# Optimization experiments

Measured on AMD Instinct MI355X. Metric: run time of the kernel, lower is better.

Reference implementation:

```python
import jax, jax.numpy as jnp
import numpy as np

HEADS = 8
DIM_HEAD = 64
SCALE = DIM_HEAD ** -0.5


def setup_inputs() -> dict:
    key = jax.random.key(0)
    ks = jax.random.split(key, 8)
    B, Nq, Nk, D = 4, 1024, 2048, 512
    inner = HEADS * DIM_HEAD  # 512
    x = jax.random.normal(ks[0], (B, Nq, D), dtype=jnp.float32)
    context = jax.random.normal(ks[1], (B, Nk, D), dtype=jnp.float32)
    bias = jax.random.normal(ks[2], (B, Nq, Nk), dtype=jnp.float32)
    s = D ** -0.5
    Wq = jax.random.normal(ks[3], (inner, D), dtype=jnp.float32) * s
    Wk = jax.random.normal(ks[4], (inner, D), dtype=jnp.float32) * s
    Wv = jax.random.normal(ks[5], (inner, D), dtype=jnp.float32) * s
    Wo = jax.random.normal(ks[6], (D, inner), dtype=jnp.float32) * s
    bo = jnp.zeros((D,), dtype=jnp.float32)
    return {"x": x, "context": context, "bias": bias,
            "Wq": Wq, "Wk": Wk, "Wv": Wv, "Wo": Wo, "bo": bo}


def reference(x, context, bias, Wq, Wk, Wv, Wo, bo):
    B, Nq, _ = x.shape
    # torch Linear: y = x @ W.T ; reshape (h d) -> b h n d
    q = (x @ Wq.T).reshape(B, Nq, HEADS, DIM_HEAD).transpose(0, 2, 1, 3)
    k = (context @ Wk.T).reshape(B, -1, HEADS, DIM_HEAD).transpose(0, 2, 1, 3)
    v = (context @ Wv.T).reshape(B, -1, HEADS, DIM_HEAD).transpose(0, 2, 1, 3)
    # explicit-score fallback path (bias supplied)
    scores = jnp.einsum('bhqd,bhkd->bhqk', q, k) * SCALE
    scores = scores + bias[:, None, :, :]  # 3D bias -> (B,1,Nq,Nk)
    attn = jax.nn.softmax(scores, axis=-1)
    out = jnp.einsum('bhqk,bhkd->bhqd', attn, v)
    out = out.transpose(0, 2, 1, 3).reshape(B, Nq, HEADS * DIM_HEAD)
    return out @ Wo.T + bo
```

## Files before the change

### kernel.cpp

```cpp
#include <hip/hip_runtime.h>

#define H 8
#define DH 64
#define NQ 1024
#define NK 2048
#define DIN 512
#define B 4
#define KSPLIT 2
#define KRANGE (NK / KSPLIT)
#define KTILES (KRANGE / 64)
#define BHNQ (B * H * NQ)

typedef __bf16 bf16;
typedef __bf16 bf16x8 __attribute__((ext_vector_type(8)));
typedef __bf16 bf16x4 __attribute__((ext_vector_type(4)));
typedef float floatx4 __attribute__((ext_vector_type(4)));

__device__ inline void gload16(const void* g, void* l) {
  __builtin_amdgcn_global_load_lds(
      (const __attribute__((address_space(1))) void*)g,
      (__attribute__((address_space(3))) void*)l, 16, 0, 0);
}

__global__ void cvt_all(const float* __restrict__ x, const float* __restrict__ ctx,
                        const float* __restrict__ wq, const float* __restrict__ wk,
                        const float* __restrict__ wv, const float* __restrict__ wo,
                        bf16* xb, bf16* cb, bf16* wqb, bf16* wkb, bf16* wvb, bf16* wob) {
  long i = ((long)blockIdx.x * 256 + threadIdx.x) * 4;
  const float* s; bf16* d; long o;
  if (i < 2097152)      { s = x;   d = xb;  o = i; }
  else if (i < 6291456) { s = ctx; d = cb;  o = i - 2097152; }
  else if (i < 6553600) { s = wq;  d = wqb; o = i - 6291456; }
  else if (i < 6815744) { s = wk;  d = wkb; o = i - 6553600; }
  else if (i < 7077888) { s = wv;  d = wvb; o = i - 6815744; }
  else                  { s = wo;  d = wob; o = i - 7077888; }
  float4 f = *(const float4*)(s + o);
  bf16x4 v = { (bf16)f.x, (bf16)f.y, (bf16)f.z, (bf16)f.w };
  *(bf16x4*)(d + o) = v;
}

__global__ __launch_bounds__(256) void gemm_qkv(
    const bf16* __restrict__ xb, const bf16* __restrict__ cb,
    const bf16* __restrict__ wqb, const bf16* __restrict__ wkb, const bf16* __restrict__ wvb,
    bf16* __restrict__ qb, bf16* __restrict__ kb, bf16* __restrict__ vtb) {
  const int which = blockIdx.z;
  if (which == 0 && blockIdx.y >= 64) return;
  const bf16* A = (which == 0) ? xb : cb;
  const bf16* W = (which == 0) ? wqb : ((which == 1) ? wkb : wvb);
  bf16* outb = (which == 0) ? qb : ((which == 1) ? kb : vtb);
  const int logT = (which == 0) ? 10 : 11;
  const float scale = (which == 0) ? 0.125f : 1.0f;
  const bool vmode = (which == 2);

  __shared__ bf16 Al[2][64 * 32];
  __shared__ bf16 Bl[2][128 * 32];
  const int t = threadIdx.x;
  const int lane = t & 63, w = t >> 6;
  const int ln = lane & 15, quad = lane >> 4;
  const int wm = (w >> 1) * 32, wn = (w & 1) * 64;
  const int rowBase = blockIdx.y * 64;
  const int colBase = blockIdx.x * 128;

  floatx4 acc[2][4] = {};
  const int rA = t >> 2, oA = (t & 3) * 8;
  const int c0 = t, c1 = t + 256;
  const int rB0 = c0 >> 2, oB0 = (c0 & 3) * 8;
  const int rB1 = c1 >> 2, oB1 = (c1 & 3) * 8;
  const bf16* Ab = A + (size_t)rowBase * DIN;
  const bf16* Wb = W + (size_t)colBase * DIN;

  gload16(Ab + (size_t)rA * DIN + oA, &Al[0][t * 8]);
  gload16(Wb + (size_t)rB0 * DIN + oB0, &Bl[0][c0 * 8]);
  gload16(Wb + (size_t)rB1 * DIN + oB1, &Bl[0][c1 * 8]);
  __syncthreads();

  for (int k0 = 0; k0 < DIN; k0 += 32) {
    const int cur = (k0 >> 5) & 1, nxt = cur ^ 1;
    if (k0 + 32 < DIN) {
      gload16(Ab + (size_t)rA * DIN + k0 + 32 + oA, &Al[nxt][t * 8]);
      gload16(Wb + (size_t)rB0 * DIN + k0 + 32 + oB0, &Bl[nxt][c0 * 8]);
      gload16(Wb + (size_t)rB1 * DIN + k0 + 32 + oB1, &Bl[nxt][c1 * 8]);
    }
    bf16x8 af[2], bfr[4];
#pragma unroll
    for (int i = 0; i < 2; i++)
      af[i] = *(const bf16x8*)&Al[cur][(wm + i * 16 + ln) * 32 + quad * 8];
#pragma unroll
    for (int j = 0; j < 4; j++)
      bfr[j] = *(const bf16x8*)&Bl[cur][(wn + j * 16 + ln) * 32 + quad * 8];
    if (!vmode) {
#pragma unroll
      for (int i = 0; i < 2; i++)
#pragma unroll
        for (int j = 0; j < 4; j++)
          acc[i][j] = __builtin_amdgcn_mfma_f32_16x16x32_bf16(af[i], bfr[j], acc[i][j], 0, 0, 0);
    } else {
#pragma unroll
      for (int i = 0; i < 2; i++)
#pragma unroll
        for (int j = 0; j < 4; j++)
          acc[i][j] = __builtin_amdgcn_mfma_f32_16x16x32_bf16(bfr[j], af[i], acc[i][j], 0, 0, 0);
    }
    __syncthreads();
  }

  const int T = 1 << logT;
#pragma unroll
  for (int i = 0; i < 2; i++)
#pragma unroll
    for (int j = 0; j < 4; j++)
#pragma unroll
      for (int r = 0; r < 4; r++) {
        if (!vmode) {
          const int m = rowBase + wm + i * 16 + quad * 4 + r;
          const int n = colBase + wn + j * 16 + ln;
          const float v = acc[i][j][r] * scale;
          const int bb = m >> logT, tok = m & (T - 1);
          const int hh = n >> 6, d = n & 63;
          outb[((((size_t)(bb * H + hh)) << logT) + tok) * DH + d] = (bf16)v;
        } else {
          const int dg = colBase + wn + j * 16 + quad * 4 + r;
          const int m = rowBase + wm + i * 16 + ln;
          const int bb = m >> logT, tok = m & (T - 1);
          const int hh = dg >> 6, d = dg & 63;
          outb[(((size_t)(bb * H + hh) * DH + d) << logT) + tok] = (bf16)acc[i][j][r];
        }
      }
}

__global__ __launch_bounds__(256) void attn_fwd(
    const bf16* __restrict__ q, const bf16* __restrict__ k,
    const bf16* __restrict__ vt, const float* __restrict__ bias,
    float* __restrict__ op0, float* __restrict__ op1, float* __restrict__ lpart) {
  __shared__ bf16 KL[64 * 64];
  __shared__ bf16 VL[64 * 64];
  __shared__ bf16 Pl[4][2][16 * 64];
  const int tid = threadIdx.x;
  const int lane = tid & 63, w = tid >> 6;
  const int ln = lane & 15, quad = lane >> 4;
  const int hh = blockIdx.y;
  const int b = blockIdx.z >> 1, ks = blockIdx.z & 1;
  const int q0 = blockIdx.x * 128;
  const int k0 = ks * KRANGE;
  const size_t bh = (size_t)b * H + hh;
  const bf16* qp = q + bh * NQ * DH;
  const bf16* kp = k + bh * NK * DH;
  const bf16* vp = vt + bh * DH * NK;
  const float* bp = bias + ((size_t)b * NQ + q0 + w * 32 + quad * 4) * NK + ln;

  bf16x8 qf[2][2];
#pragma unroll
  for (int s = 0; s < 2; s++)
#pragma unroll
    for (int kc = 0; kc < 2; kc++)
      qf[s][kc] = *(const bf16x8*)(qp + (size_t)(q0 + w * 32 + s * 16 + ln) * DH + kc * 32 + quad * 8);

  floatx4 o[2][4] = {};
  floatx4 lac[2] = {};
  const bf16x8 ones = {(bf16)1.f, (bf16)1.f, (bf16)1.f, (bf16)1.f,
                       (bf16)1.f, (bf16)1.f, (bf16)1.f, (bf16)1.f};
  constexpr float L2E = 1.44269504f;
  constexpr float OFF = 34.6246810f;

  for (int tt = 0; tt < KTILES; tt++) {
    const int nk0 = k0 + tt * 64;
#pragma unroll
    for (int s = 0; s < 2; s++) {
      const int i = s * 256 + tid;
      const int sr = i >> 3, sc = (i & 7) ^ (sr & 7);
      gload16(kp + (size_t)(nk0 + sr) * DH + sc * 8, &KL[i * 8]);
      gload16(vp + (size_t)sr * NK + nk0 + sc * 8, &VL[i * 8]);
    }
    float bc[2][4][4];
#pragma unroll
    for (int s = 0; s < 2; s++)
#pragma unroll
      for (int j = 0; j < 4; j++)
#pragma unroll
        for (int r = 0; r < 4; r++)
          bc[s][j][r] = bp[(size_t)(s * 16 + r) * NK + nk0 + j * 16];
    __syncthreads();

    floatx4 s4[2][4];
#pragma unroll
    for (int s = 0; s < 2; s++)
#pragma unroll
      for (int j = 0; j < 4; j++) {
        s4[s][j][0] = bc[s][j][0]; s4[s][j][1] = bc[s][j][1];
        s4[s][j][2] = bc[s][j][2]; s4[s][j][3] = bc[s][j][3];
      }
#pragma unroll
    for (int j = 0; j < 4; j++)
#pragma unroll
      for (int kc = 0; kc < 2; kc++) {
        const int kr = j * 16 + ln;
        bf16x8 kf = *(const bf16x8*)&KL[kr * 64 + (((kc * 4 + quad) ^ (kr & 7)) * 8)];
        s4[0][j] = __builtin_amdgcn_mfma_f32_16x16x32_bf16(qf[0][kc], kf, s4[0][j], 0, 0, 0);
        s4[1][j] = __builtin_amdgcn_mfma_f32_16x16x32_bf16(qf[1][kc], kf, s4[1][j], 0, 0, 0);
      }

#pragma unroll
    for (int s = 0; s < 2; s++)
#pragma unroll
      for (int j = 0; j < 4; j++)
#pragma unroll
        for (int r = 0; r < 4; r++)
          s4[s][j][r] = exp2f(fmaf(s4[s][j][r], L2E, -OFF));

#pragma unroll
    for (int s = 0; s < 2; s++)
#pragma unroll
      for (int j = 0; j < 4; j++)
#pragma unroll
        for (int r = 0; r < 4; r++) {
          const int m = quad * 4 + r;
          Pl[w][s][m * 64 + (((j * 2 + (ln >> 3)) ^ (m & 7)) * 8) + (ln & 7)] = (bf16)s4[s][j][r];
        }
    asm volatile("s_waitcnt lgkmcnt(0)" ::: "memory");
    bf16x8 pf[2][2];
#pragma unroll
    for (int s = 0; s < 2; s++)
#pragma unroll
      for (int kc = 0; kc < 2; kc++)
        pf[s][kc] = *(const bf16x8*)&Pl[w][s][ln * 64 + (((kc * 4 + quad) ^ (ln & 7)) * 8)];

#pragma unroll
    for (int s = 0; s < 2; s++)
#pragma unroll
      for (int kc = 0; kc < 2; kc++)
        lac[s] = __builtin_amdgcn_mfma_f32_16x16x32_bf16(pf[s][kc], ones, lac[s], 0, 0, 0);

#pragma unroll
    for (int jn = 0; jn < 4; jn++)
#pragma unroll
      for (int kc = 0; kc < 2; kc++) {
        const int vr = jn * 16 + ln;
        bf16x8 vf = *(const bf16x8*)&VL[vr * 64 + (((kc * 4 + quad) ^ (vr & 7)) * 8)];
        o[0][jn] = __builtin_amdgcn_mfma_f32_16x16x32_bf16(pf[0][kc], vf, o[0][jn], 0, 0, 0);
        o[1][jn] = __builtin_amdgcn_mfma_f32_16x16x32_bf16(pf[1][kc], vf, o[1][jn], 0, 0, 0);
      }
    __syncthreads();
  }

#pragma unroll
  for (int s = 0; s < 2; s++) {
    float* op = (ks ? op1 : op0) +
                ((size_t)b * NQ + q0 + w * 32 + s * 16 + quad * 4) * DIN + hh * 64 + ln;
#pragma unroll
    for (int jn = 0; jn < 4; jn++)
#pragma unroll
      for (int r = 0; r < 4; r++)
        op[(size_t)r * DIN + jn * 16] = o[s][jn][r];
    if (ln == 0) {
      float4 lv = {lac[s][0], lac[s][1], lac[s][2], lac[s][3]};
      *(float4*)&lpart[((size_t)ks * B * H + b * H + hh) * NQ + q0 + w * 32 + s * 16 + quad * 4] = lv;
    }
  }
}

__global__ __launch_bounds__(256) void gemm_out(
    const float* __restrict__ op0, const float* __restrict__ op1,
    const float* __restrict__ lp, const bf16* __restrict__ W,
    float* __restrict__ outf, const float* __restrict__ bo) {
  __shared__ bf16 Al[2][64 * 32];
  __shared__ bf16 Bl[2][128 * 32];
  const int t = threadIdx.x;
  const int lane = t & 63, w = t >> 6;
  const int ln = lane & 15, quad = lane >> 4;
  const int wm = (w >> 1) * 32, wn = (w & 1) * 64;
  const int rowBase = blockIdx.y * 64;
  const int colBase = blockIdx.x * 128;

  floatx4 acc[2][4] = {};
  const int rA = t >> 2, oA = (t & 3) * 8;
  const int c0 = t, c1 = t + 256;
  const int rB0 = c0 >> 2, oB0 = (c0 & 3) * 8;
  const int rB1 = c1 >> 2, oB1 = (c1 & 3) * 8;
  const int m0 = rowBase + rA;
  const bf16* Wb = W + (size_t)colBase * DIN;

  float linv0[8];
#pragma unroll
  for (int h = 0; h < 8; h++) {
    const int i0 = ((m0 >> 10) * H + h) * NQ + (m0 & 1023);
    linv0[h] = 1.0f / (lp[i0] + lp[BHNQ + i0]);
  }

#define STAGE_A(K0V, BUF)                                                      \
  {                                                                            \
    const float sA = linv0[(K0V) >> 6];                                        \
    const float* pa0 = op0 + (size_t)m0 * DIN + (K0V) + oA;                    \
    const float* pa1 = op1 + (size_t)m0 * DIN + (K0V) + oA;                    \
    float4 xa = *(const float4*)pa0, xb2 = *(const float4*)(pa0 + 4);          \
    float4 ya = *(const float4*)pa1, yb = *(const float4*)(pa1 + 4);           \
    bf16x8 v0 = {(bf16)((xa.x + ya.x) * sA), (bf16)((xa.y + ya.y) * sA),       \
                 (bf16)((xa.z + ya.z) * sA), (bf16)((xa.w + ya.w) * sA),       \
                 (bf16)((xb2.x + yb.x) * sA), (bf16)((xb2.y + yb.y) * sA),     \
                 (bf16)((xb2.z + yb.z) * sA), (bf16)((xb2.w + yb.w) * sA)};    \
    *(bf16x8*)&Al[BUF][t * 8] = v0;                                            \
  }

  STAGE_A(0, 0);
  gload16(Wb + (size_t)rB0 * DIN + oB0, &Bl[0][c0 * 8]);
  gload16(Wb + (size_t)rB1 * DIN + oB1, &Bl[0][c1 * 8]);
  __syncthreads();

#pragma unroll
  for (int kk = 0; kk < 16; kk++) {
    const int cur = kk & 1, nxt = cur ^ 1;
    if (kk < 15) {
      const int k1 = (kk + 1) * 32;
      STAGE_A(k1, nxt);
      gload16(Wb + (size_t)rB0 * DIN + k1 + oB0, &Bl[nxt][c0 * 8]);
      gload16(Wb + (size_t)rB1 * DIN + k1 + oB1, &Bl[nxt][c1 * 8]);
    }
    bf16x8 af[2], bfr[4];
#pragma unroll
    for (int i = 0; i < 2; i++)
      af[i] = *(const bf16x8*)&Al[cur][(wm + i * 16 + ln) * 32 + quad * 8];
#pragma unroll
    for (int j = 0; j < 4; j++)
      bfr[j] = *(const bf16x8*)&Bl[cur][(wn + j * 16 + ln) * 32 + quad * 8];
#pragma unroll
    for (int i = 0; i < 2; i++)
#pragma unroll
      for (int j = 0; j < 4; j++)
        acc[i][j] = __builtin_amdgcn_mfma_f32_16x16x32_bf16(af[i], bfr[j], acc[i][j], 0, 0, 0);
    __syncthreads();
  }
#undef STAGE_A

#pragma unroll
  for (int i = 0; i < 2; i++)
#pragma unroll
    for (int j = 0; j < 4; j++)
#pragma unroll
      for (int r = 0; r < 4; r++) {
        const int m = rowBase + wm + i * 16 + quad * 4 + r;
        const int n = colBase + wn + j * 16 + ln;
        outf[(size_t)m * DIN + n] = acc[i][j][r] + bo[n];
      }
}

extern "C" void kernel_launch(void* const* d_in, const int* in_sizes, int n_in,
                              void* d_out, int out_size, void* d_ws, size_t ws_size,
                              hipStream_t stream) {
  const float* x    = (const float*)d_in[0];
  const float* ctx  = (const float*)d_in[1];
  const float* bias = (const float*)d_in[2];
  const float* Wq   = (const float*)d_in[3];
  const float* Wk   = (const float*)d_in[4];
  const float* Wv   = (const float*)d_in[5];
  const float* Wo   = (const float*)d_in[6];
  const float* bo   = (const float*)d_in[7];
  float* out = (float*)d_out;

  char* p = (char*)d_ws;
  bf16* xb   = (bf16*)(p + 0);
  bf16* cb   = (bf16*)(p + 4194304);
  bf16* wqb  = (bf16*)(p + 12582912);
  bf16* wkb  = (bf16*)(p + 13107200);
  bf16* wvb  = (bf16*)(p + 13631488);
  bf16* wob  = (bf16*)(p + 14155776);
  bf16* qb   = (bf16*)(p + 14680064);
  bf16* kb   = (bf16*)(p + 18874368);
  bf16* vtb  = (bf16*)(p + 27262976);
  float* op1 = (float*)(p + 35651584);
  float* lpart = (float*)(p + 44040192);
  float* op0 = (float*)cb;

  cvt_all<<<7168, 256, 0, stream>>>(x, ctx, Wq, Wk, Wv, Wo, xb, cb, wqb, wkb, wvb, wob);
  gemm_qkv<<<dim3(4, 128, 3), 256, 0, stream>>>(xb, cb, wqb, wkb, wvb, qb, kb, vtb);
  attn_fwd<<<dim3(NQ / 128, H, B * KSPLIT), 256, 0, stream>>>(qb, kb, vtb, bias, op0, op1, lpart);
  gemm_out<<<dim3(4, 64), 256, 0, stream>>>(op0, op1, lpart, wob, out, bo);
}
```

Baseline: 192.5 us.

## Transpose attention MFMA operands for vectorized bias loads and P stores

Swaps the A/B operands of the QK^T and PV MFMAs so each lane holds four consecutive key columns (and output dims) per query row. This lets bias be read as float4 vectors, P be written to LDS as bf16x4 instead of scalar bf16 stores, and the output be stored as float4. It also uses the hardware exp2 builtin directly. The change cuts scalar memory instructions in the attention inner loop, at the cost of a new swizzle layout that must stay bank-conflict free.

New measurement: 192.1 us. About the same (-0.3%).

```diff
diff --git a/kernel.cpp b/kernel.cpp
--- a/kernel.cpp
+++ b/kernel.cpp
@@ -20,6 +20,14 @@
   __builtin_amdgcn_global_load_lds(
       (const __attribute__((address_space(1))) void*)g,
       (__attribute__((address_space(3))) void*)l, 16, 0, 0);
+}
+
+__device__ inline float fexp2(float x) {
+#if __has_builtin(__builtin_amdgcn_exp2f)
+  return __builtin_amdgcn_exp2f(x);
+#else
+  return exp2f(x);
+#endif
 }
 
 __global__ void cvt_all(const float* __restrict__ x, const float* __restrict__ ctx,
@@ -134,7 +142,7 @@
     float* __restrict__ op0, float* __restrict__ op1, float* __restrict__ lpart) {
   __shared__ bf16 KL[64 * 64];
   __shared__ bf16 VL[64 * 64];
-  __shared__ bf16 Pl[4][2][16 * 64];
+  __shared__ __attribute__((aligned(16))) bf16 Pl[4][2][16][64];
   const int tid = threadIdx.x;
   const int lane = tid & 63, w = tid >> 6;
   const int ln = lane & 15, quad = lane >> 4;
@@ -146,7 +154,8 @@
   const bf16* qp = q + bh * NQ * DH;
   const bf16* kp = k + bh * NK * DH;
   const bf16* vp = vt + bh * DH * NK;
-  const float* bp = bias + ((size_t)b * NQ + q0 + w * 32 + quad * 4) * NK + ln;
+  const float* bp0 = bias + ((size_t)b * NQ + q0 + w * 32 + ln) * NK + k0 + quad * 4;
+  const float* bp1 = bp0 + (size_t)16 * NK;
 
   bf16x8 qf[2][2];
 #pragma unroll
@@ -171,64 +180,52 @@
       gload16(kp + (size_t)(nk0 + sr) * DH + sc * 8, &KL[i * 8]);
       gload16(vp + (size_t)sr * NK + nk0 + sc * 8, &VL[i * 8]);
     }
-    float bc[2][4][4];
-#pragma unroll
-    for (int s = 0; s < 2; s++)
-#pragma unroll
-      for (int j = 0; j < 4; j++)
-#pragma unroll
-        for (int r = 0; r < 4; r++)
-          bc[s][j][r] = bp[(size_t)(s * 16 + r) * NK + nk0 + j * 16];
+    floatx4 s4[2][4];
+#pragma unroll
+    for (int j = 0; j < 4; j++) {
+      s4[0][j] = *(const floatx4*)(bp0 + tt * 64 + j * 16);
+      s4[1][j] = *(const floatx4*)(bp1 + tt * 64 + j * 16);
+    }
     __syncthreads();
 
-    floatx4 s4[2][4];
-#pragma unroll
-    for (int s = 0; s < 2; s++)
-#pragma unroll
-      for (int j = 0; j < 4; j++) {
-        s4[s][j][0] = bc[s][j][0]; s4[s][j][1] = bc[s][j][1];
-        s4[s][j][2] = bc[s][j][2]; s4[s][j][3] = bc[s][j][3];
-      }
 #pragma unroll
     for (int j = 0; j < 4; j++)
 #pragma unroll
       for (int kc = 0; kc < 2; kc++) {
         const int kr = j * 16 + ln;
         bf16x8 kf = *(const bf16x8*)&KL[kr * 64 + (((kc * 4 + quad) ^ (kr & 7)) * 8)];
-        s4[0][j] = __builtin_amdgcn_mfma_f32_16x16x32_bf16(qf[0][kc], kf, s4[0][j], 0, 0, 0);
-        s4[1][j] = __builtin_amdgcn_mfma_f32_16x16x32_bf16(qf[1][kc], kf, s4[1][j], 0, 0, 0);
+        s4[0][j] = __builtin_amdgcn_mfma_f32_16x16x32_bf16(kf, qf[0][kc], s4[0][j], 0, 0, 0);
+        s4[1][j] = __builtin_amdgcn_mfma_f32_16x16x32_bf16(kf, qf[1][kc], s4[1][j], 0, 0, 0);
       }
 
 #pragma unroll
     for (int s = 0; s < 2; s++)
 #pragma unroll
-      for (int j = 0; j < 4; j++)
-#pragma unroll
-        for (int r = 0; r < 4; r++)
-          s4[s][j][r] = exp2f(fmaf(s4[s][j][r], L2E, -OFF));
-
+      for (int j = 0; j < 4; j++) {
+        const float e0 = fexp2(fmaf(s4[s][j][0], L2E, -OFF));
+        const float e1 = fexp2(fmaf(s4[s][j][1], L2E, -OFF));
+        const float e2 = fexp2(fmaf(s4[s][j][2], L2E, -OFF));
+        const float e3 = fexp2(fmaf(s4[s][j][3], L2E, -OFF));
+        bf16x4 pv4 = {(bf16)e0, (bf16)e1, (bf16)e2, (bf16)e3};
+        const int tok = (j * 16 + quad * 4) ^ ((ln & 7) << 3);
+        *(bf16x4*)&Pl[w][s][ln][tok] = pv4;
+      }
+    asm volatile("s_waitcnt lgkmcnt(0)" ::: "memory");
+
+    bf16x8 pt[2][2];
 #pragma unroll
     for (int s = 0; s < 2; s++)
 #pragma unroll
-      for (int j = 0; j < 4; j++)
-#pragma unroll
-        for (int r = 0; r < 4; r++) {
-          const int m = quad * 4 + r;
-          Pl[w][s][m * 64 + (((j * 2 + (ln >> 3)) ^ (m & 7)) * 8) + (ln & 7)] = (bf16)s4[s][j][r];
-        }
-    asm volatile("s_waitcnt lgkmcnt(0)" ::: "memory");
-    bf16x8 pf[2][2];
+      for (int kc = 0; kc < 2; kc++) {
+        const int tok = (kc * 32 + quad * 8) ^ ((ln & 7) << 3);
+        pt[s][kc] = *(const bf16x8*)&Pl[w][s][ln][tok];
+      }
+
 #pragma unroll
     for (int s = 0; s < 2; s++)
 #pragma unroll
       for (int kc = 0; kc < 2; kc++)
-        pf[s][kc] = *(const bf16x8*)&Pl[w][s][ln * 64 + (((kc * 4 + quad) ^ (ln & 7)) * 8)];
-
-#pragma unroll
-    for (int s = 0; s < 2; s++)
-#pragma unroll
-      for (int kc = 0; kc < 2; kc++)
-        lac[s] = __builtin_amdgcn_mfma_f32_16x16x32_bf16(pf[s][kc], ones, lac[s], 0, 0, 0);
+        lac[s] = __builtin_amdgcn_mfma_f32_16x16x32_bf16(ones, pt[s][kc], lac[s], 0, 0, 0);
 
 #pragma unroll
     for (int jn = 0; jn < 4; jn++)
@@ -236,8 +233,8 @@
       for (int kc = 0; kc < 2; kc++) {
         const int vr = jn * 16 + ln;
         bf16x8 vf = *(const bf16x8*)&VL[vr * 64 + (((kc * 4 + quad) ^ (vr & 7)) * 8)];
-        o[0][jn] = __builtin_amdgcn_mfma_f32_16x16x32_bf16(pf[0][kc], vf, o[0][jn], 0, 0, 0);
-        o[1][jn] = __builtin_amdgcn_mfma_f32_16x16x32_bf16(pf[1][kc], vf, o[1][jn], 0, 0, 0);
+        o[0][jn] = __builtin_amdgcn_mfma_f32_16x16x32_bf16(vf, pt[0][kc], o[0][jn], 0, 0, 0);
+        o[1][jn] = __builtin_amdgcn_mfma_f32_16x16x32_bf16(vf, pt[1][kc], o[1][jn], 0, 0, 0);
       }
     __syncthreads();
   }
@@ -245,16 +242,12 @@
 #pragma unroll
   for (int s = 0; s < 2; s++) {
     float* op = (ks ? op1 : op0) +
-                ((size_t)b * NQ + q0 + w * 32 + s * 16 + quad * 4) * DIN + hh * 64 + ln;
+                ((size_t)b * NQ + q0 + w * 32 + s * 16 + ln) * DIN + hh * 64 + quad * 4;
 #pragma unroll
     for (int jn = 0; jn < 4; jn++)
-#pragma unroll
-      for (int r = 0; r < 4; r++)
-        op[(size_t)r * DIN + jn * 16] = o[s][jn][r];
-    if (ln == 0) {
-      float4 lv = {lac[s][0], lac[s][1], lac[s][2], lac[s][3]};
-      *(float4*)&lpart[((size_t)ks * B * H + b * H + hh) * NQ + q0 + w * 32 + s * 16 + quad * 4] = lv;
-    }
+      *(floatx4*)(op + jn * 16) = o[s][jn];
+    if (quad == 0)
+      lpart[((size_t)ks * B * H + b * H + hh) * NQ + q0 + w * 32 + s * 16 + ln] = lac[s][0];
   }
 }
 
```
